# Kernel tuning notes

Hardware: AMD Instinct MI355X
Metric: run time of the kernel (lower is better)

## Reference

```python
import jax, jax.numpy as jnp
import numpy as np

PROP_TIME = 3
# (top,bottom),(left,right) zero-pad widths for the 8 neighbor shifts,
# matching torch ZeroPad2d((left,right,top,bottom)) in the original module.
PADS = [((0, 2), (0, 2)), ((0, 2), (1, 1)), ((0, 2), (2, 0)),
        ((1, 1), (0, 2)),                   ((1, 1), (2, 0)),
        ((2, 0), (0, 2)), ((2, 0), (1, 1)), ((2, 0), (2, 0))]


def _pad8(x, axis):
    """Pad last two dims 8 ways, stack the copies on `axis`."""
    lead = [(0, 0)] * (x.ndim - 2)
    return jnp.stack([jnp.pad(x, lead + [tb, lr]) for (tb, lr) in PADS], axis=axis)


def _affinity_norm(g):
    # g: [N, 8, H, W] -> gate_wb [N, 8, H+2, W+2], gate_sum [N, H, W]
    gw = jnp.stack([jnp.pad(g[:, k], [(0, 0), PADS[k][0], PADS[k][1]])
                    for k in range(8)], axis=1)
    abs_w = jnp.sum(jnp.abs(gw), axis=1, keepdims=True)
    gw = gw / abs_w
    gsum = jnp.sum(gw, axis=1)[:, 1:-1, 1:-1]
    return gw, gsum


def _propagate_once(gw, gsum, blur):
    # gw: [N,8,H+2,W+2], gsum: [N,H,W], blur: [N,B,H,W]
    nb = _pad8(blur, axis=1)                                # [N,8,B,H+2,W+2]
    ws = jnp.sum(gw[:, :, None] * nb, axis=1)[:, :, 1:-1, 1:-1]  # [N,B,H,W]
    return (1.0 - gsum[:, None]) * blur + ws


def _forward(guidance, blur, prop_time):
    # guidance: [24, X, Y, Z], blur: [B, X, Y, Z]
    gwx, gsx = _affinity_norm(jnp.transpose(guidance[0:8],   (3, 0, 1, 2)))  # [Z,8,X,Y]
    gwy, gsy = _affinity_norm(jnp.transpose(guidance[8:16],  (2, 0, 1, 3)))  # [Y,8,X,Z]
    gwz, gsz = _affinity_norm(jnp.transpose(guidance[16:24], (1, 0, 2, 3)))  # [X,8,Y,Z]
    r = blur
    for _ in range(prop_time):
        r = jnp.transpose(_propagate_once(gwx, gsx, jnp.transpose(r, (3, 0, 1, 2))), (1, 2, 3, 0))
        r = jnp.transpose(_propagate_once(gwy, gsy, jnp.transpose(r, (2, 0, 1, 3))), (1, 2, 0, 3))
        r = jnp.transpose(_propagate_once(gwz, gsz, jnp.transpose(r, (1, 0, 2, 3))), (1, 0, 2, 3))
    return r


def setup_inputs() -> dict:
    key = jax.random.key(0)
    k1, k2 = jax.random.split(key)
    guidance = jax.random.normal(k1, (24, 256, 256, 32), dtype=jnp.float32)
    blur = jax.random.normal(k2, (1, 256, 256, 32), dtype=jnp.float32)
    return {"guidance": guidance, "blur": blur}


def reference(guidance, blur):
    return _forward(guidance, blur, PROP_TIME)
```

## Files before the change

### kernel.cpp

```cpp
#include <hip/hip_runtime.h>
#include <hip/hip_fp16.h>


constexpr int NV = 256 * 256 * 32;
constexpr int YZ = 256 * 32;
constexpr int NG = NV / 4;
constexpr int GEND = 24 * NV;

constexpr int TXB = 8, TYB = 16;
constexpr int RX = 12, RY = 20;
constexpr int NCOL = RX * RY;
constexpr int CSTR = 36;
constexpr int LOFF = 16;
constexpr int LSZ = NCOL * CSTR + 2 * LOFF;

struct alignas(16) H8 { __half2 h[4]; };

__device__ __forceinline__ int iclamp(int v, int lo, int hi) {
    return min(max(v, lo), hi);
}

__device__ __forceinline__ void unpack8(const H8& r, float* w) {
    float2 f;
    f = __half22float2(r.h[0]); w[0] = f.x; w[1] = f.y;
    f = __half22float2(r.h[1]); w[2] = f.x; w[3] = f.y;
    f = __half22float2(r.h[2]); w[4] = f.x; w[5] = f.y;
    f = __half22float2(r.h[3]); w[6] = f.x; w[7] = f.y;
}

template <int DIR>
__device__ __forceinline__ void wgroup_t(int f0, const float* __restrict__ g,
                                         H8* __restrict__ wt) {
    constexpr int d1[8] = {1, 1, 1, 0, 0, -1, -1, -1};
    constexpr int d2[8] = {1, 0, -1, 1, -1, 1, 0, -1};
    const int z = f0 & 31, y = (f0 >> 5) & 255, x = f0 >> 13;
    const int gb0 = DIR * 8 * NV;

    float G[8][4];

    if (DIR == 0) {
#pragma unroll
        for (int k = 0; k < 8; ++k) {
            const int a = x + d1[k], b = y + d2[k];
            const bool valid = ((unsigned)a < 256u) & ((unsigned)b < 256u);
            const int ofs = f0 + d1[k] * YZ + d2[k] * 32;
            float4 gv = *(const float4*)(g + iclamp(gb0 + k * NV + ofs, 0, GEND - 4));
            if (!valid) { gv.x = 0.f; gv.y = 0.f; gv.z = 0.f; gv.w = 0.f; }
            G[k][0] = gv.x; G[k][1] = gv.y; G[k][2] = gv.z; G[k][3] = gv.w;
        }
    } else {
        const int s1 = (DIR == 1) ? YZ : 32;
        const int c1 = (DIR == 1) ? x : y;
        const bool zlo = (z > 0), zhi = (z < 28);
#pragma unroll
        for (int k = 0; k < 8; ++k) {
            const bool vrow = (unsigned)(c1 + d1[k]) < 256u;
            const int gb = gb0 + k * NV + f0 + d1[k] * s1;
            float4 gv = *(const float4*)(g + iclamp(gb, 0, GEND - 4));
            if (!vrow) { gv.x = 0.f; gv.y = 0.f; gv.z = 0.f; gv.w = 0.f; }
            if (d2[k] == 1) {
                float ge = g[iclamp(gb + 4, 0, GEND - 1)];
                ge = (vrow && zhi) ? ge : 0.f;
                G[k][0] = gv.y; G[k][1] = gv.z; G[k][2] = gv.w; G[k][3] = ge;
            } else if (d2[k] == -1) {
                float ge = g[iclamp(gb - 1, 0, GEND - 1)];
                ge = (vrow && zlo) ? ge : 0.f;
                G[k][0] = ge; G[k][1] = gv.x; G[k][2] = gv.y; G[k][3] = gv.z;
            } else {
                G[k][0] = gv.x; G[k][1] = gv.y; G[k][2] = gv.z; G[k][3] = gv.w;
            }
        }
    }

#pragma unroll
    for (int i = 0; i < 4; ++i) {
        float asum = 0.f;
#pragma unroll
        for (int k = 0; k < 8; ++k) asum += fabsf(G[k][i]);
        const float winv = __builtin_amdgcn_rcpf(asum);
        H8 rec;
#pragma unroll
        for (int p = 0; p < 4; ++p)
            rec.h[p] = __floats2half2_rn(G[2 * p][i] * winv, G[2 * p + 1][i] * winv);
        const int zz = (f0 + i) & 31;
        wt[((DIR * 32 + zz) << 16) + (x << 8) + y] = rec;
    }
}

__global__ __launch_bounds__(256) void make_w(const float* __restrict__ g,
                                              H8* __restrict__ wt) {
    const int b = blockIdx.x;
    const int dir = b >> 11;
    const int f0 = ((b & 2047) * 256 + threadIdx.x) << 2;
    if (dir == 0)      wgroup_t<0>(f0, g, wt);
    else if (dir == 1) wgroup_t<1>(f0, g, wt);
    else               wgroup_t<2>(f0, g, wt);
}

template <int DIR, bool STORE>
__device__ __forceinline__ void fstep(const H8* __restrict__ wt,
                                      const float* __restrict__ src,
                                      float* __restrict__ dst,
                                      float* __restrict__ gq,
                                      int cb, int gxc, int gyc, bool in) {
    if (!in) return;
    const H8* wp = wt + ((DIR * 32) << 16) + (gxc << 8) + gyc;

#pragma unroll
    for (int zb = 0; zb < 32; zb += 4) {
        H8 wr[4];
#pragma unroll
        for (int i = 0; i < 4; ++i) wr[i] = wp[(zb + i) << 16];

        float out4[4];
        if (DIR == 0) {
            constexpr int ofs[8] = {RY + 1, RY, RY - 1, 1, -1, -(RY - 1), -RY, -(RY + 1)};
            const float4 vc = *(const float4*)(src + cb + zb);
            const float rc4[4] = {vc.x, vc.y, vc.z, vc.w};
            float nb[8][4];
#pragma unroll
            for (int k = 0; k < 8; ++k) {
                const float4 v = *(const float4*)(src + cb + zb + ofs[k] * CSTR);
                nb[k][0] = v.x; nb[k][1] = v.y; nb[k][2] = v.z; nb[k][3] = v.w;
            }
#pragma unroll
            for (int i = 0; i < 4; ++i) {
                float w[8]; unpack8(wr[i], w);
                float a = rc4[i];
#pragma unroll
                for (int k = 0; k < 8; ++k) a = fmaf(w[k], nb[k][i] - rc4[i], a);
                out4[i] = a;
            }
        } else {
            constexpr int S = (DIR == 1) ? RY : 1;
            float v[3][4], lo[3], hi[3];
#pragma unroll
            for (int j = 0; j < 3; ++j) {
                const int cofs = cb + zb + (1 - j) * S * CSTR;
                const float4 t4 = *(const float4*)(src + cofs);
                v[j][0] = t4.x; v[j][1] = t4.y; v[j][2] = t4.z; v[j][3] = t4.w;
                lo[j] = src[cofs - 1];
                hi[j] = src[cofs + 4];
            }
#pragma unroll
            for (int i = 0; i < 4; ++i) {
                float w[8]; unpack8(wr[i], w);
                const float rc  = v[1][i];
                const float zp0 = (i < 3) ? v[0][i + 1] : hi[0];
                const float zm0 = (i > 0) ? v[0][i - 1] : lo[0];
                const float zp1 = (i < 3) ? v[1][i + 1] : hi[1];
                const float zm1 = (i > 0) ? v[1][i - 1] : lo[1];
                const float zp2 = (i < 3) ? v[2][i + 1] : hi[2];
                const float zm2 = (i > 0) ? v[2][i - 1] : lo[2];
                float a = rc;
                a = fmaf(w[0], zp0 - rc, a);
                a = fmaf(w[1], v[0][i] - rc, a);
                a = fmaf(w[2], zm0 - rc, a);
                a = fmaf(w[3], zp1 - rc, a);
                a = fmaf(w[4], zm1 - rc, a);
                a = fmaf(w[5], zp2 - rc, a);
                a = fmaf(w[6], v[2][i] - rc, a);
                a = fmaf(w[7], zm2 - rc, a);
                out4[i] = a;
            }
        }
        const float4 o = make_float4(out4[0], out4[1], out4[2], out4[3]);
        if (STORE) *(float4*)(gq + zb) = o;
        else       *(float4*)(dst + cb + zb) = o;
    }
}

__global__ __launch_bounds__(256) void iter3(const H8* __restrict__ wt,
                                             const float* __restrict__ rin,
                                             float* __restrict__ rout) {
    __shared__ float A[LSZ];
    __shared__ float B[LSZ];
    const int t  = threadIdx.x;
    const int bx = blockIdx.x & 31, by = blockIdx.x >> 5;
    const bool act = t < NCOL;
    const int rx = t / RY, ry = t - rx * RY;
    const int gx = bx * TXB - 2 + rx, gy = by * TYB - 2 + ry;
    const int gxc = iclamp(gx, 0, 255), gyc = iclamp(gy, 0, 255);
    const int cb = t * CSTR + LOFF;

    for (int i = t; i < LSZ; i += 256) { A[i] = 0.f; B[i] = 0.f; }
    __syncthreads();
    if (act) {
        const float* p = rin + ((gxc << 8) + gyc) * 32;
#pragma unroll
        for (int j = 0; j < 8; ++j)
            *(float4*)(A + cb + 4 * j) = *(const float4*)(p + 4 * j);
    }
    __syncthreads();

    const bool in0 = act && rx >= 1 && rx <= RX - 2 && ry >= 1 && ry <= RY - 2;
    const bool in1 = act && rx >= 2 && rx <= RX - 3 && ry >= 1 && ry <= RY - 2;
    const bool in2 = act && rx >= 2 && rx <= RX - 3 && ry >= 2 && ry <= RY - 3;

    fstep<0, false>(wt, A, B, nullptr, cb, gxc, gyc, in0);
    __syncthreads();
    fstep<1, false>(wt, B, A, nullptr, cb, gxc, gyc, in1);
    __syncthreads();
    float* gq = rout + ((gx << 8) + gy) * 32;
    fstep<2, true>(wt, A, nullptr, gq, cb, gxc, gyc, in2);
}

template <int DIR>
__global__ __launch_bounds__(256) void prop_step(const float* __restrict__ g,
                                                 const float* __restrict__ rin,
                                                 float* __restrict__ rout) {
    constexpr int d1[8] = {1, 1, 1, 0, 0, -1, -1, -1};
    constexpr int d2[8] = {1, 0, -1, 1, -1, 1, 0, -1};
    const int t = blockIdx.x * 256 + threadIdx.x;
    const int f0 = t << 2;
    const int z = f0 & 31, y = (f0 >> 5) & 255, x = f0 >> 13;
    const int gb0 = DIR * 8 * NV;

    float as[4] = {0, 0, 0, 0}, ac[4] = {0, 0, 0, 0};
    float4 rc;

    if (DIR == 0) {
        rc = *(const float4*)(rin + f0);
#pragma unroll
        for (int k = 0; k < 8; ++k) {
            const int a = x + d1[k], b = y + d2[k];
            const bool valid = ((unsigned)a < 256u) & ((unsigned)b < 256u);
            const int ofs = f0 + d1[k] * YZ + d2[k] * 32;
            const float4 rv = *(const float4*)(rin + iclamp(ofs, 0, NV - 4));
            float4 gv = *(const float4*)(g + iclamp(gb0 + k * NV + ofs, 0, GEND - 4));
            if (!valid) { gv.x = 0.f; gv.y = 0.f; gv.z = 0.f; gv.w = 0.f; }
            as[0] += fabsf(gv.x); as[1] += fabsf(gv.y);
            as[2] += fabsf(gv.z); as[3] += fabsf(gv.w);
            ac[0] = fmaf(gv.x, rv.x - rc.x, ac[0]); ac[1] = fmaf(gv.y, rv.y - rc.y, ac[1]);
            ac[2] = fmaf(gv.z, rv.z - rc.z, ac[2]); ac[3] = fmaf(gv.w, rv.w - rc.w, ac[3]);
        }
    } else {
        const int s1 = (DIR == 1) ? YZ : 32;
        const int c1 = (DIR == 1) ? x : y;
        float4 rv[3]; float rl[3], rr[3];
#pragma unroll
        for (int j = 0; j < 3; ++j) {
            const int ro = f0 + (1 - j) * s1;
            rv[j] = *(const float4*)(rin + iclamp(ro, 0, NV - 4));
            rl[j] = rin[iclamp(ro - 1, 0, NV - 1)];
            rr[j] = rin[iclamp(ro + 4, 0, NV - 1)];
        }
        rc = rv[1];
        const bool zlo = (z > 0), zhi = (z < 28);
#pragma unroll
        for (int k = 0; k < 8; ++k) {
            const int j = 1 - d1[k];
            const bool vrow = (unsigned)(c1 + d1[k]) < 256u;
            const int gb = gb0 + k * NV + f0 + d1[k] * s1;
            float4 gv = *(const float4*)(g + iclamp(gb, 0, GEND - 4));
            if (!vrow) { gv.x = 0.f; gv.y = 0.f; gv.z = 0.f; gv.w = 0.f; }
            float4 gk, rk;
            if (d2[k] == 1) {
                float ge = g[iclamp(gb + 4, 0, GEND - 1)];
                ge = (vrow && zhi) ? ge : 0.f;
                gk = make_float4(gv.y, gv.z, gv.w, ge);
                rk = make_float4(rv[j].y, rv[j].z, rv[j].w, rr[j]);
            } else if (d2[k] == -1) {
                float ge = g[iclamp(gb - 1, 0, GEND - 1)];
                ge = (vrow && zlo) ? ge : 0.f;
                gk = make_float4(ge, gv.x, gv.y, gv.z);
                rk = make_float4(rl[j], rv[j].x, rv[j].y, rv[j].z);
            } else {
                gk = gv; rk = rv[j];
            }
            as[0] += fabsf(gk.x); as[1] += fabsf(gk.y);
            as[2] += fabsf(gk.z); as[3] += fabsf(gk.w);
            ac[0] = fmaf(gk.x, rk.x - rc.x, ac[0]); ac[1] = fmaf(gk.y, rk.y - rc.y, ac[1]);
            ac[2] = fmaf(gk.z, rk.z - rc.z, ac[2]); ac[3] = fmaf(gk.w, rk.w - rc.w, ac[3]);
        }
    }

    float4 o;
    o.x = rc.x + ac[0] * __builtin_amdgcn_rcpf(as[0]);
    o.y = rc.y + ac[1] * __builtin_amdgcn_rcpf(as[1]);
    o.z = rc.z + ac[2] * __builtin_amdgcn_rcpf(as[2]);
    o.w = rc.w + ac[3] * __builtin_amdgcn_rcpf(as[3]);
    *(float4*)(rout + f0) = o;
}

extern "C" void kernel_launch(void* const* d_in, const int* in_sizes, int n_in,
                              void* d_out, int out_size, void* d_ws, size_t ws_size,
                              hipStream_t stream) {
    const float* g    = (const float*)d_in[0];
    const float* blur = (const float*)d_in[1];
    float* out = (float*)d_out;

    const size_t WBYTES = (size_t)3 * NV * sizeof(H8);
    const size_t NEED   = WBYTES + (size_t)2 * NV * sizeof(float);

    if (ws_size >= NEED) {
        H8*    wt   = (H8*)d_ws;
        float* bufA = (float*)((char*)d_ws + WBYTES);
        float* bufB = bufA + NV;

        make_w<<<dim3(3 * NG / 256), dim3(256), 0, stream>>>(g, wt);
        iter3<<<dim3(512), dim3(256), 0, stream>>>(wt, blur, bufA);
        iter3<<<dim3(512), dim3(256), 0, stream>>>(wt, bufA, bufB);
        iter3<<<dim3(512), dim3(256), 0, stream>>>(wt, bufB, out);
    } else {
        float* ws = (float*)d_ws;
        const dim3 block(256), sgrid(NG / 256);
        const float* src = blur;
        for (int step = 0; step < 9; ++step) {
            float* dst = (step & 1) ? ws : out;
            switch (step % 3) {
                case 0: prop_step<0><<<sgrid, block, 0, stream>>>(g, src, dst); break;
                case 1: prop_step<1><<<sgrid, block, 0, stream>>>(g, src, dst); break;
                case 2: prop_step<2><<<sgrid, block, 0, stream>>>(g, src, dst); break;
            }
            src = dst;
        }
    }
}
```

Baseline: 360.7 us.

## Replace fused shared-memory three-step tile kernel with nine per-direction global stencil kernels

Removes the fused iter3 kernel, which ran all three directional steps inside one block using shared-memory tiles with halo recompute. It is replaced by nine separate launches of a simple per-element global-memory stencil kernel. The weight table layout also changes from z-major planes to the natural element order, so each thread reads its four weights contiguously. This drops the halo overhead and the barriers, but the intermediate field now makes a round trip through global memory on every step and the launch count triples.

```diff
diff --git a/kernel.cpp b/kernel.cpp
--- a/kernel.cpp
+++ b/kernel.cpp
@@ -6,13 +6,6 @@
 constexpr int YZ = 256 * 32;
 constexpr int NG = NV / 4;
 constexpr int GEND = 24 * NV;
-
-constexpr int TXB = 8, TYB = 16;
-constexpr int RX = 12, RY = 20;
-constexpr int NCOL = RX * RY;
-constexpr int CSTR = 36;
-constexpr int LOFF = 16;
-constexpr int LSZ = NCOL * CSTR + 2 * LOFF;
 
 struct alignas(16) H8 { __half2 h[4]; };
 
@@ -82,8 +75,7 @@
 #pragma unroll
         for (int p = 0; p < 4; ++p)
             rec.h[p] = __floats2half2_rn(G[2 * p][i] * winv, G[2 * p + 1][i] * winv);
-        const int zz = (f0 + i) & 31;
-        wt[((DIR * 32 + zz) << 16) + (x << 8) + y] = rec;
+        wt[DIR * NV + f0 + i] = rec;
     }
 }
 
@@ -97,112 +89,58 @@
     else               wgroup_t<2>(f0, g, wt);
 }
 
-template <int DIR, bool STORE>
-__device__ __forceinline__ void fstep(const H8* __restrict__ wt,
-                                      const float* __restrict__ src,
-                                      float* __restrict__ dst,
-                                      float* __restrict__ gq,
-                                      int cb, int gxc, int gyc, bool in) {
-    if (!in) return;
-    const H8* wp = wt + ((DIR * 32) << 16) + (gxc << 8) + gyc;
-
-#pragma unroll
-    for (int zb = 0; zb < 32; zb += 4) {
-        H8 wr[4];
-#pragma unroll
-        for (int i = 0; i < 4; ++i) wr[i] = wp[(zb + i) << 16];
-
-        float out4[4];
-        if (DIR == 0) {
-            constexpr int ofs[8] = {RY + 1, RY, RY - 1, 1, -1, -(RY - 1), -RY, -(RY + 1)};
-            const float4 vc = *(const float4*)(src + cb + zb);
-            const float rc4[4] = {vc.x, vc.y, vc.z, vc.w};
-            float nb[8][4];
-#pragma unroll
-            for (int k = 0; k < 8; ++k) {
-                const float4 v = *(const float4*)(src + cb + zb + ofs[k] * CSTR);
-                nb[k][0] = v.x; nb[k][1] = v.y; nb[k][2] = v.z; nb[k][3] = v.w;
-            }
-#pragma unroll
-            for (int i = 0; i < 4; ++i) {
-                float w[8]; unpack8(wr[i], w);
-                float a = rc4[i];
-#pragma unroll
-                for (int k = 0; k < 8; ++k) a = fmaf(w[k], nb[k][i] - rc4[i], a);
-                out4[i] = a;
-            }
-        } else {
-            constexpr int S = (DIR == 1) ? RY : 1;
-            float v[3][4], lo[3], hi[3];
-#pragma unroll
-            for (int j = 0; j < 3; ++j) {
-                const int cofs = cb + zb + (1 - j) * S * CSTR;
-                const float4 t4 = *(const float4*)(src + cofs);
-                v[j][0] = t4.x; v[j][1] = t4.y; v[j][2] = t4.z; v[j][3] = t4.w;
-                lo[j] = src[cofs - 1];
-                hi[j] = src[cofs + 4];
-            }
-#pragma unroll
-            for (int i = 0; i < 4; ++i) {
-                float w[8]; unpack8(wr[i], w);
-                const float rc  = v[1][i];
-                const float zp0 = (i < 3) ? v[0][i + 1] : hi[0];
-                const float zm0 = (i > 0) ? v[0][i - 1] : lo[0];
-                const float zp1 = (i < 3) ? v[1][i + 1] : hi[1];
-                const float zm1 = (i > 0) ? v[1][i - 1] : lo[1];
-                const float zp2 = (i < 3) ? v[2][i + 1] : hi[2];
-                const float zm2 = (i > 0) ? v[2][i - 1] : lo[2];
-                float a = rc;
-                a = fmaf(w[0], zp0 - rc, a);
-                a = fmaf(w[1], v[0][i] - rc, a);
-                a = fmaf(w[2], zm0 - rc, a);
-                a = fmaf(w[3], zp1 - rc, a);
-                a = fmaf(w[4], zm1 - rc, a);
-                a = fmaf(w[5], zp2 - rc, a);
-                a = fmaf(w[6], v[2][i] - rc, a);
-                a = fmaf(w[7], zm2 - rc, a);
-                out4[i] = a;
-            }
-        }
-        const float4 o = make_float4(out4[0], out4[1], out4[2], out4[3]);
-        if (STORE) *(float4*)(gq + zb) = o;
-        else       *(float4*)(dst + cb + zb) = o;
-    }
-}
-
-__global__ __launch_bounds__(256) void iter3(const H8* __restrict__ wt,
+template <int DIR>
+__global__ __launch_bounds__(256) void wstep(const H8* __restrict__ wt,
                                              const float* __restrict__ rin,
                                              float* __restrict__ rout) {
-    __shared__ float A[LSZ];
-    __shared__ float B[LSZ];
-    const int t  = threadIdx.x;
-    const int bx = blockIdx.x & 31, by = blockIdx.x >> 5;
-    const bool act = t < NCOL;
-    const int rx = t / RY, ry = t - rx * RY;
-    const int gx = bx * TXB - 2 + rx, gy = by * TYB - 2 + ry;
-    const int gxc = iclamp(gx, 0, 255), gyc = iclamp(gy, 0, 255);
-    const int cb = t * CSTR + LOFF;
-
-    for (int i = t; i < LSZ; i += 256) { A[i] = 0.f; B[i] = 0.f; }
-    __syncthreads();
-    if (act) {
-        const float* p = rin + ((gxc << 8) + gyc) * 32;
-#pragma unroll
-        for (int j = 0; j < 8; ++j)
-            *(float4*)(A + cb + 4 * j) = *(const float4*)(p + 4 * j);
-    }
-    __syncthreads();
-
-    const bool in0 = act && rx >= 1 && rx <= RX - 2 && ry >= 1 && ry <= RY - 2;
-    const bool in1 = act && rx >= 2 && rx <= RX - 3 && ry >= 1 && ry <= RY - 2;
-    const bool in2 = act && rx >= 2 && rx <= RX - 3 && ry >= 2 && ry <= RY - 3;
-
-    fstep<0, false>(wt, A, B, nullptr, cb, gxc, gyc, in0);
-    __syncthreads();
-    fstep<1, false>(wt, B, A, nullptr, cb, gxc, gyc, in1);
-    __syncthreads();
-    float* gq = rout + ((gx << 8) + gy) * 32;
-    fstep<2, true>(wt, A, nullptr, gq, cb, gxc, gyc, in2);
+    constexpr int d1[8] = {1, 1, 1, 0, 0, -1, -1, -1};
+    constexpr int d2[8] = {1, 0, -1, 1, -1, 1, 0, -1};
+    const int t = blockIdx.x * 256 + threadIdx.x;
+    const int f0 = t << 2;
+
+    const H8* wp = wt + DIR * NV + f0;
+    float w[4][8];
+#pragma unroll
+    for (int i = 0; i < 4; ++i) unpack8(wp[i], w[i]);
+
+    float a[4];
+
+    if (DIR == 0) {
+        const float4 rc = *(const float4*)(rin + f0);
+        const float rc4[4] = {rc.x, rc.y, rc.z, rc.w};
+        a[0] = rc.x; a[1] = rc.y; a[2] = rc.z; a[3] = rc.w;
+#pragma unroll
+        for (int k = 0; k < 8; ++k) {
+            const int ofs = f0 + d1[k] * YZ + d2[k] * 32;
+            const float4 rv = *(const float4*)(rin + iclamp(ofs, 0, NV - 4));
+            const float nb[4] = {rv.x, rv.y, rv.z, rv.w};
+#pragma unroll
+            for (int i = 0; i < 4; ++i)
+                a[i] = fmaf(w[i][k], nb[i] - rc4[i], a[i]);
+        }
+    } else {
+        constexpr int s1 = (DIR == 1) ? YZ : 32;
+        float e[3][6];
+#pragma unroll
+        for (int j = 0; j < 3; ++j) {
+            const int ro = f0 + (1 - j) * s1;
+            const float4 rv = *(const float4*)(rin + iclamp(ro, 0, NV - 4));
+            e[j][0] = rin[iclamp(ro - 1, 0, NV - 1)];
+            e[j][1] = rv.x; e[j][2] = rv.y; e[j][3] = rv.z; e[j][4] = rv.w;
+            e[j][5] = rin[iclamp(ro + 4, 0, NV - 1)];
+        }
+        const float rc4[4] = {e[1][1], e[1][2], e[1][3], e[1][4]};
+        a[0] = rc4[0]; a[1] = rc4[1]; a[2] = rc4[2]; a[3] = rc4[3];
+#pragma unroll
+        for (int k = 0; k < 8; ++k) {
+            const int j = 1 - d1[k];
+#pragma unroll
+            for (int i = 0; i < 4; ++i)
+                a[i] = fmaf(w[i][k], e[j][1 + i + d2[k]] - rc4[i], a[i]);
+        }
+    }
+
+    *(float4*)(rout + f0) = make_float4(a[0], a[1], a[2], a[3]);
 }
 
 template <int DIR>
@@ -299,9 +237,17 @@
         float* bufB = bufA + NV;
 
         make_w<<<dim3(3 * NG / 256), dim3(256), 0, stream>>>(g, wt);
-        iter3<<<dim3(512), dim3(256), 0, stream>>>(wt, blur, bufA);
-        iter3<<<dim3(512), dim3(256), 0, stream>>>(wt, bufA, bufB);
-        iter3<<<dim3(512), dim3(256), 0, stream>>>(wt, bufB, out);
+
+        const float* src = blur;
+        for (int step = 0; step < 9; ++step) {
+            float* dst = (step == 8) ? out : ((step & 1) ? bufB : bufA);
+            switch (step % 3) {
+                case 0: wstep<0><<<dim3(NG / 256), dim3(256), 0, stream>>>(wt, src, dst); break;
+                case 1: wstep<1><<<dim3(NG / 256), dim3(256), 0, stream>>>(wt, src, dst); break;
+                case 2: wstep<2><<<dim3(NG / 256), dim3(256), 0, stream>>>(wt, src, dst); break;
+            }
+            src = dst;
+        }
     } else {
         float* ws = (float*)d_ws;
         const dim3 block(256), sgrid(NG / 256);
```

Measured after the change: 389.3 us. 7.9% more time.
